# Performance work log

Hardware: AMD Instinct MI355X
Metric: run time of the kernel (lower is better)

## Reference

```python
import jax, jax.numpy as jnp
import numpy as np

D = 768       # model dim
H = 8         # heads
DH = 96       # dim per head
M = 256       # FAVOR+ random features
DEPTH = 6
B = 8
NM = 4        # n_masks
FF = 3072     # 4*dim feedforward
N = 512       # tokens = (1024/16)*(128/16)


def setup_inputs() -> dict:
    key = jax.random.key(0)
    ks = jax.random.split(key, 16)
    g = lambda k, shape: jax.random.normal(k, shape, jnp.float32) * 0.02
    return {
        "mel": jax.random.normal(ks[0], (B, 1, 1024, 128), jnp.float32),
        "patch_w": g(ks[1], (D, 1, 16, 16)),
        "patch_b": jnp.zeros((D,), jnp.float32),
        "pos_embed": g(ks[2], (1, N, D)),
        "proj": jax.random.normal(ks[3], (M, DH), jnp.float32),  # FAVOR+ projection (buffer, no grad)
        "ln1_s": jnp.ones((DEPTH, D)), "ln1_b": jnp.zeros((DEPTH, D)),
        "qkv_w": g(ks[4], (DEPTH, D, 3 * D)), "qkv_b": jnp.zeros((DEPTH, 3 * D)),
        "ao_w": g(ks[5], (DEPTH, D, D)), "ao_b": jnp.zeros((DEPTH, D)),
        "ln2_s": jnp.ones((DEPTH, D)), "ln2_b": jnp.zeros((DEPTH, D)),
        "ff1_w": g(ks[6], (DEPTH, D, FF)), "ff1_b": jnp.zeros((DEPTH, FF)),
        "ff2_w": g(ks[7], (DEPTH, FF, D)), "ff2_b": jnp.zeros((DEPTH, D)),
        "mask_w": g(ks[8], (D, NM)), "mask_b": jnp.zeros((NM,), jnp.float32),
    }


def _ln(x, s, b):
    mu = x.mean(-1, keepdims=True)
    v = ((x - mu) ** 2).mean(-1, keepdims=True)
    return (x - mu) / jnp.sqrt(v + 1e-5) * s + b


def _phi(x, proj, is_query):
    # FAVOR+ softmax-kernel feature map. x: (b,h,n,d), proj: (m,d)
    xd = x * (x.shape[-1] ** -0.25)            # d^{-1/4} data normalizer
    u = jnp.einsum('bhnd,md->bhnm', xd, proj)
    diag = 0.5 * jnp.sum(xd * xd, axis=-1, keepdims=True)
    stab = jnp.max(u, axis=-1, keepdims=True) if is_query else jnp.max(u)
    stab = jax.lax.stop_gradient(stab)          # matches .detach() in performer
    return (jnp.exp(u - diag - stab) + 1e-4) * (proj.shape[0] ** -0.5)


def reference(mel, patch_w, patch_b, pos_embed, proj, ln1_s, ln1_b, qkv_w, qkv_b,
              ao_w, ao_b, ln2_s, ln2_b, ff1_w, ff1_b, ff2_w, ff2_b, mask_w, mask_b):
    # --- frozen AudioMAE patch embed (+pos embed), under no_grad in torch ---
    x = jax.lax.conv_general_dilated(mel, patch_w, (16, 16), 'VALID',
                                     dimension_numbers=('NCHW', 'OIHW', 'NCHW'))  # (B,D,64,8)
    b = x.shape[0]
    x = x.reshape(b, D, -1).transpose(0, 2, 1) + patch_b  # (B,N,D)
    x = x + pos_embed
    x = jax.lax.stop_gradient(x)
    proj = jax.lax.stop_gradient(proj)

    def heads(t):
        return t.reshape(b, -1, H, DH).transpose(0, 2, 1, 3)  # (b,h,n,dh)

    for l in range(DEPTH):
        # --- FAVOR+ linear attention block ---
        h = _ln(x, ln1_s[l], ln1_b[l])
        qkv = h @ qkv_w[l] + qkv_b[l]
        q, k, v = (heads(t) for t in jnp.split(qkv, 3, axis=-1))
        pq = _phi(q, proj, True)
        pk = _phi(k, proj, False)
        ctx = jnp.einsum('bhnm,bhne->bhme', pk, v)       # (b,h,m,dh) linear-time kv summary
        out = jnp.einsum('bhnm,bhme->bhne', pq, ctx)
        den = jnp.einsum('bhnm,bhm->bhn', pq, pk.sum(axis=2))
        out = out / den[..., None]
        out = out.transpose(0, 2, 1, 3).reshape(b, -1, D)
        x = x + out @ ao_w[l] + ao_b[l]
        # --- feedforward block ---
        h = _ln(x, ln2_s[l], ln2_b[l])
        h = jax.nn.gelu(h @ ff1_w[l] + ff1_b[l], approximate=False)
        x = x + h @ ff2_w[l] + ff2_b[l]

    logits = x @ mask_w + mask_b              # (B,N,M)
    masks = jax.nn.sigmoid(logits)
    return masks.transpose(0, 2, 1)           # (B,M,N)
```

## Files before the change

### kernel.cpp

```cpp
#include <hip/hip_runtime.h>
#include <hip/hip_bf16.h>

typedef __bf16 bf16;
typedef __bf16 bf16x8 __attribute__((ext_vector_type(8)));
typedef float f32x4 __attribute__((ext_vector_type(4)));
typedef unsigned int u32;

#define PHI_SCALE  0.31947154f
#define DIAG_SCALE 0.05103104f
#define FEAT_SCALE 0.0625f

__device__ __forceinline__ void glds16(const bf16* g, bf16* l) {
  __builtin_amdgcn_global_load_lds(
      (const __attribute__((address_space(1))) u32*)g,
      (__attribute__((address_space(3))) u32*)l, 16, 0, 0);
}

__device__ __forceinline__ void xcd_remap(int& bx, int& by) {
  int nbx = gridDim.x, nby = gridDim.y;
  int lin = bx + nbx * by;
  int xcd = lin & 7, idx = lin >> 3;
  int mloc = nbx >> 2, nloc = nby >> 1;
  int xm = xcd & 3, xn = xcd >> 2;
  bx = xm * mloc + (idx % mloc);
  by = xn * nloc + (idx / mloc);
}

__device__ __forceinline__ int swz_scol(int lane) {
  return (((lane & 3) ^ ((lane >> 3) & 3)) * 8);
}

__device__ __forceinline__ float waveSum(float v) {
#pragma unroll
  for (int o = 32; o > 0; o >>= 1) v += __shfl_xor(v, o, 64);
  return v;
}
__device__ __forceinline__ float waveMax(float v) {
#pragma unroll
  for (int o = 32; o > 0; o >>= 1) v = fmaxf(v, __shfl_xor(v, o, 64));
  return v;
}
__device__ __forceinline__ float blockSum(float v) {
  __shared__ float tmp[4];
  v = waveSum(v);
  if ((threadIdx.x & 63) == 0) tmp[threadIdx.x >> 6] = v;
  __syncthreads();
  float r = tmp[0] + tmp[1] + tmp[2] + tmp[3];
  __syncthreads();
  return r;
}
__device__ __forceinline__ float blockMax(float v) {
  __shared__ float tmp[4];
  v = waveMax(v);
  if ((threadIdx.x & 63) == 0) tmp[threadIdx.x >> 6] = v;
  __syncthreads();
  float r = fmaxf(fmaxf(tmp[0], tmp[1]), fmaxf(tmp[2], tmp[3]));
  __syncthreads();
  return r;
}

__global__ __launch_bounds__(256) void patches_kernel(const float* __restrict__ mel,
    bf16* __restrict__ patches) {
  int blk = blockIdx.x, t = threadIdx.x;
  int b = blk >> 9, n = blk & 511;
  int r0 = (n >> 3) << 4, c0 = (n & 7) << 4;
  patches[(size_t)blk * 256 + t] =
      (bf16)mel[((size_t)b * 1024 + r0 + (t >> 4)) * 128 + c0 + (t & 15)];
}

__global__ __launch_bounds__(256) void cvt_kernel(const float* __restrict__ src,
    bf16* __restrict__ dst, int n) {
  int i = blockIdx.x * 256 + threadIdx.x;
  if (i < n) dst[i] = (bf16)src[i];
}

__device__ __forceinline__ void tile_transpose(const float* __restrict__ src,
    bf16* __restrict__ dst, int K, int N, int bx, int by) {
  __shared__ float lds[64][65];
  int n0 = bx * 64, k0 = by * 64;
  int t = threadIdx.x;
  for (int idx = t; idx < 4096; idx += 256) {
    int r = idx >> 6, c = idx & 63;
    lds[r][c] = src[(size_t)(k0 + r) * N + n0 + c];
  }
  __syncthreads();
  for (int idx = t; idx < 4096; idx += 256) {
    int r = idx >> 6, c = idx & 63;
    dst[(size_t)(n0 + r) * K + k0 + c] = (bf16)lds[c][r];
  }
}
__global__ __launch_bounds__(256) void transpose4_kernel(
    const float* __restrict__ w0, bf16* __restrict__ d0,
    const float* __restrict__ w1, bf16* __restrict__ d1,
    const float* __restrict__ w2, bf16* __restrict__ d2,
    const float* __restrict__ w3, bf16* __restrict__ d3) {
  int i = blockIdx.x;
  if (i < 432)       { tile_transpose(w0, d0, 768, 2304, i % 36, i / 36); }
  else if (i < 576)  { i -= 432;  tile_transpose(w1, d1, 768, 768, i % 12, i / 12); }
  else if (i < 1152) { i -= 576;  tile_transpose(w2, d2, 768, 3072, i % 48, i / 48);}
  else               { i -= 1152; tile_transpose(w3, d3, 3072, 768, i % 12, i / 12);}
}

__global__ __launch_bounds__(256) void ln_kernel(const float* __restrict__ x,
    const float* __restrict__ s, const float* __restrict__ bta, bf16* __restrict__ h) {
  int row = blockIdx.x;
  const float* xr = x + (size_t)row * 768;
  int t = threadIdx.x;
  float v0 = xr[t], v1 = xr[t + 256], v2 = xr[t + 512];
  float mu = blockSum(v0 + v1 + v2) * (1.f / 768.f);
  float d0 = v0 - mu, d1 = v1 - mu, d2 = v2 - mu;
  float var = blockSum(d0 * d0 + d1 * d1 + d2 * d2) * (1.f / 768.f);
  float inv = rsqrtf(var + 1e-5f);
  bf16* hr = h + (size_t)row * 768;
  hr[t]       = (bf16)(d0 * inv * s[t]       + bta[t]);
  hr[t + 256] = (bf16)(d1 * inv * s[t + 256] + bta[t + 256]);
  hr[t + 512] = (bf16)(d2 * inv * s[t + 512] + bta[t + 512]);
}

__global__ __launch_bounds__(256) void gemm128(const bf16* __restrict__ A,
    const bf16* __restrict__ B, const float* __restrict__ bias,
    bf16* __restrict__ outb, int N, int K, int mode) {
  __shared__ __attribute__((aligned(16))) bf16 lds_a[2 * 128 * 32];
  __shared__ __attribute__((aligned(16))) bf16 lds_b[2 * 128 * 32];
  int bx = blockIdx.x, by = blockIdx.y;
  xcd_remap(bx, by);
  const int t = threadIdx.x;
  const int m0 = bx * 128, n0 = by * 128;
  const int wave = t >> 6, lane = t & 63;
  const int quad = lane >> 4, id = lane & 15;
  const int wr = wave >> 1, wc = wave & 1;
  const int srow = lane >> 2, scol = swz_scol(lane);
  const bf16* pa0 = A + (size_t)(m0 + wave * 32 + srow) * K + scol;
  const bf16* pa1 = pa0 + (size_t)16 * K;
  const bf16* pb0 = B + (size_t)(n0 + wave * 32 + srow) * K + scol;
  const bf16* pb1 = pb0 + (size_t)16 * K;
  bf16* la = lds_a + wave * 1024;
  bf16* lb = lds_b + wave * 1024;
  const int sl = (quad ^ ((id >> 1) & 3)) * 8;
  f32x4 acc[4][4] = {};
  for (int k0 = 0; k0 < K; k0 += 64) {
    glds16(pa0, la);      glds16(pa1, la + 512);
    glds16(pa0 + 32, la + 4096); glds16(pa1 + 32, la + 4096 + 512);
    glds16(pb0, lb);      glds16(pb1, lb + 512);
    glds16(pb0 + 32, lb + 4096); glds16(pb1 + 32, lb + 4096 + 512);
    pa0 += 64; pa1 += 64; pb0 += 64; pb1 += 64;
    __syncthreads();
#pragma unroll
    for (int kh = 0; kh < 2; kh++) {
      bf16x8 af[4], bg[4];
#pragma unroll
      for (int i = 0; i < 4; i++)
        af[i] = *(bf16x8*)&lds_a[kh * 4096 + (wr * 64 + i * 16 + id) * 32 + sl];
#pragma unroll
      for (int j = 0; j < 4; j++)
        bg[j] = *(bf16x8*)&lds_b[kh * 4096 + (wc * 64 + j * 16 + id) * 32 + sl];
#pragma unroll
      for (int i = 0; i < 4; i++)
#pragma unroll
        for (int j = 0; j < 4; j++)
          acc[i][j] = __builtin_amdgcn_mfma_f32_16x16x32_bf16(af[i], bg[j], acc[i][j], 0, 0, 0);
    }
    __syncthreads();
  }
#pragma unroll
  for (int i = 0; i < 4; i++) {
#pragma unroll
    for (int j = 0; j < 4; j++) {
#pragma unroll
      for (int r = 0; r < 4; r++) {
        int rr = m0 + wr * 64 + i * 16 + quad * 4 + r;
        int cc = n0 + wc * 64 + j * 16 + id;
        float v = acc[i][j][r] + bias[cc];
        if (mode == 1) v = 0.5f * v * (1.0f + erff(v * 0.70710678f));
        outb[(size_t)rr * N + cc] = (bf16)v;
      }
    }
  }
}

__global__ __launch_bounds__(256) void gemm_b64(const bf16* __restrict__ A,
    const bf16* __restrict__ B, const float* __restrict__ bias,
    bf16* __restrict__ outb, float* __restrict__ xout,
    const float* __restrict__ pos, int N, int kchunk, int mode) {
  __shared__ __attribute__((aligned(16))) bf16 lds_a[2 * 128 * 32];
  __shared__ __attribute__((aligned(16))) bf16 lds_b[2 * 64 * 32];
  int bx = blockIdx.x, by = blockIdx.y;
  xcd_remap(bx, by);
  const int t = threadIdx.x;
  const int m0 = bx * 128, n0 = by * 64;
  const int kz = blockIdx.z;
  const int k_start = kz * kchunk;
  const int wave = t >> 6, lane = t & 63;
  const int quad = lane >> 4, id = lane & 15;
  const int srow = lane >> 2, scol = swz_scol(lane);
  const int K = kchunk * gridDim.z;
  const bf16* pa0 = A + (size_t)(m0 + wave * 32 + srow) * K + k_start + scol;
  const bf16* pa1 = pa0 + (size_t)16 * K;
  const bf16* pb  = B + (size_t)(n0 + wave * 16 + srow) * K + k_start + scol;
  bf16* la = lds_a + wave * 1024;
  bf16* lb = lds_b + wave * 512;
  const int sl = (quad ^ ((id >> 1) & 3)) * 8;
  f32x4 acc[2][4] = {};
  for (int k0 = 0; k0 < kchunk; k0 += 64) {
    glds16(pa0, la);      glds16(pa1, la + 512);
    glds16(pa0 + 32, la + 4096); glds16(pa1 + 32, la + 4096 + 512);
    glds16(pb, lb);       glds16(pb + 32, lb + 2048);
    pa0 += 64; pa1 += 64; pb += 64;
    __syncthreads();
#pragma unroll
    for (int kh = 0; kh < 2; kh++) {
      bf16x8 af[2], bg[4];
#pragma unroll
      for (int i = 0; i < 2; i++)
        af[i] = *(bf16x8*)&lds_a[kh * 4096 + (wave * 32 + i * 16 + id) * 32 + sl];
#pragma unroll
      for (int j = 0; j < 4; j++)
        bg[j] = *(bf16x8*)&lds_b[kh * 2048 + (j * 16 + id) * 32 + sl];
#pragma unroll
      for (int i = 0; i < 2; i++)
#pragma unroll
        for (int j = 0; j < 4; j++)
          acc[i][j] = __builtin_amdgcn_mfma_f32_16x16x32_bf16(af[i], bg[j], acc[i][j], 0, 0, 0);
    }
    __syncthreads();
  }
#pragma unroll
  for (int i = 0; i < 2; i++) {
#pragma unroll
    for (int j = 0; j < 4; j++) {
#pragma unroll
      for (int r = 0; r < 4; r++) {
        int rr = m0 + wave * 32 + i * 16 + quad * 4 + r;
        int cc = n0 + j * 16 + id;
        if (mode == 4) {
          float v = acc[i][j][r] + (kz == 0 ? bias[cc] : 0.f);
          atomicAdd(&xout[(size_t)rr * N + cc], v);
        } else {
          float v = acc[i][j][r] + bias[cc];
          if (mode == 0) {
            outb[(size_t)rr * N + cc] = (bf16)v;
          } else if (mode == 1) {
            outb[(size_t)rr * N + cc] = (bf16)(0.5f * v * (1.0f + erff(v * 0.70710678f)));
          } else {
            xout[(size_t)rr * N + cc] = v + pos[(size_t)(rr & 511) * 768 + cc];
          }
        }
      }
    }
  }
}

__global__ __launch_bounds__(256) void phi_q_kernel(const bf16* __restrict__ qkv,
    const bf16* __restrict__ proj, bf16* __restrict__ pq) {
  __shared__ __attribute__((aligned(16))) bf16 lA[3][64 * 32];
  __shared__ __attribute__((aligned(16))) bf16 lB[3][256 * 32];
  __shared__ float sqlds[64];
  const int t = threadIdx.x;
  const int nt = blockIdx.x, bh = blockIdx.y;
  const int b = bh >> 3, h = bh & 7;
  const int n0 = nt * 64;
  const bf16* Abase = qkv + ((size_t)(b * 512 + n0)) * 2304 + h * 96;
#pragma unroll
  for (int c = 0; c < 3; c++) {
    int v = c * 256 + t;
    int row = v / 12, s = v % 12;
    *(bf16x8*)&lA[s >> 2][row * 32 + (s & 3) * 8] = *(const bf16x8*)&Abase[(size_t)row * 2304 + s * 8];
  }
#pragma unroll
  for (int c = 0; c < 12; c++) {
    int v = c * 256 + t;
    int row = v / 12, s = v % 12;
    *(bf16x8*)&lB[s >> 2][row * 32 + (s & 3) * 8] = *(const bf16x8*)&proj[(size_t)row * 96 + s * 8];
  }
  __syncthreads();
  const int wave = t >> 6, lane = t & 63, quad = lane >> 4, id = lane & 15;
  f32x4 acc[16] = {};
  float sq = 0.f;
#pragma unroll
  for (int kb = 0; kb < 3; kb++) {
    bf16x8 af = *(bf16x8*)&lA[kb][(wave * 16 + id) * 32 + quad * 8];
#pragma unroll
    for (int e = 0; e < 8; e++) { float fv = (float)af[e]; sq += fv * fv; }
#pragma unroll
    for (int j = 0; j < 16; j++) {
      bf16x8 bg = *(bf16x8*)&lB[kb][(j * 16 + id) * 32 + quad * 8];
      acc[j] = __builtin_amdgcn_mfma_f32_16x16x32_bf16(af, bg, acc[j], 0, 0, 0);
    }
  }
  sq += __shfl_xor(sq, 16, 64);
  sq += __shfl_xor(sq, 32, 64);
  if (quad == 0) sqlds[wave * 16 + id] = sq;
  __syncthreads();
#pragma unroll
  for (int r = 0; r < 4; r++) {
    int rrow = quad * 4 + r;
    float dg = DIAG_SCALE * sqlds[wave * 16 + rrow];
    float mx = -1e30f;
#pragma unroll
    for (int j = 0; j < 16; j++) mx = fmaxf(mx, acc[j][r]);
    mx = fmaxf(mx, __shfl_xor(mx, 1, 64));
    mx = fmaxf(mx, __shfl_xor(mx, 2, 64));
    mx = fmaxf(mx, __shfl_xor(mx, 4, 64));
    mx = fmaxf(mx, __shfl_xor(mx, 8, 64));
    float umax = mx * PHI_SCALE;
#pragma unroll
    for (int j = 0; j < 16; j++) {
      float uu = acc[j][r] * PHI_SCALE;
      float val = (expf(uu - dg - umax) + 1e-4f) * FEAT_SCALE;
      pq[((size_t)bh * 512 + n0 + wave * 16 + rrow) * 256 + j * 16 + id] = (bf16)val;
    }
  }
}

__global__ __launch_bounds__(256) void phi_k_kernel(const bf16* __restrict__ qkv,
    const bf16* __restrict__ proj, bf16* __restrict__ prov, float* __restrict__ kbm) {
  __shared__ __attribute__((aligned(16))) bf16 lA[3][64 * 32];
  __shared__ __attribute__((aligned(16))) bf16 lB[3][256 * 32];
  __shared__ float sqlds[64];
  __shared__ float bmax4[4];
  const int t = threadIdx.x;
  const int nt = blockIdx.x, bh = blockIdx.y;
  const int b = bh >> 3, h = bh & 7;
  const int n0 = nt * 64;
  const bf16* Abase = qkv + ((size_t)(b * 512 + n0)) * 2304 + 768 + h * 96;
#pragma unroll
  for (int c = 0; c < 3; c++) {
    int v = c * 256 + t;
    int row = v / 12, s = v % 12;
    *(bf16x8*)&lA[s >> 2][row * 32 + (s & 3) * 8] = *(const bf16x8*)&Abase[(size_t)row * 2304 + s * 8];
  }
#pragma unroll
  for (int c = 0; c < 12; c++) {
    int v = c * 256 + t;
    int row = v / 12, s = v % 12;
    *(bf16x8*)&lB[s >> 2][row * 32 + (s & 3) * 8] = *(const bf16x8*)&proj[(size_t)row * 96 + s * 8];
  }
  __syncthreads();
  const int wave = t >> 6, lane = t & 63, quad = lane >> 4, id = lane & 15;
  f32x4 acc[16] = {};
  float sq = 0.f;
#pragma unroll
  for (int kb = 0; kb < 3; kb++) {
    bf16x8 af = *(bf16x8*)&lA[kb][(wave * 16 + id) * 32 + quad * 8];
#pragma unroll
    for (int e = 0; e < 8; e++) { float fv = (float)af[e]; sq += fv * fv; }
#pragma unroll
    for (int j = 0; j < 16; j++) {
      bf16x8 bg = *(bf16x8*)&lB[kb][(j * 16 + id) * 32 + quad * 8];
      acc[j] = __builtin_amdgcn_mfma_f32_16x16x32_bf16(af, bg, acc[j], 0, 0, 0);
    }
  }
  sq += __shfl_xor(sq, 16, 64);
  sq += __shfl_xor(sq, 32, 64);
  if (quad == 0) sqlds[wave * 16 + id] = sq;
  float bm = -1e30f;
#pragma unroll
  for (int j = 0; j < 16; j++)
#pragma unroll
    for (int r = 0; r < 4; r++) bm = fmaxf(bm, acc[j][r]);
  bm = waveMax(bm);
  if (lane == 0) bmax4[wave] = bm;
  __syncthreads();
  float blkmax = fmaxf(fmaxf(bmax4[0], bmax4[1]), fmaxf(bmax4[2], bmax4[3])) * PHI_SCALE;
  if (t == 0) kbm[bh * 8 + nt] = blkmax;
#pragma unroll
  for (int r = 0; r < 4; r++) {
    int rrow = quad * 4 + r;
    float dg = DIAG_SCALE * sqlds[wave * 16 + rrow];
#pragma unroll
    for (int j = 0; j < 16; j++) {
      float uu = acc[j][r] * PHI_SCALE;
      prov[((size_t)bh * 512 + n0 + wave * 16 + rrow) * 256 + j * 16 + id] =
          (bf16)expf(uu - dg - blkmax);
    }
  }
}

__global__ __launch_bounds__(256) void pkt_kernel(const bf16* __restrict__ prov,
    const float* __restrict__ kbm, bf16* __restrict__ pkT) {
  __shared__ bf16 lds[64][65];
  const int m0 = blockIdx.x * 64, nt = blockIdx.y, bh = blockIdx.z;
  const int n0 = nt * 64;
  const int t = threadIdx.x;
  float gmax = blockMax(fmaxf(kbm[t], kbm[t + 256]));
  float factor = expf(kbm[bh * 8 + nt] - gmax);
  const bf16* src = prov + ((size_t)bh * 512 + n0) * 256 + m0;
#pragma unroll
  for (int c = 0; c < 16; c++) {
    int idx = c * 256 + t; int r = idx >> 6, cc = idx & 63;
    float pv = (float)src[(size_t)r * 256 + cc];
    lds[cc][r] = (bf16)((pv * factor + 1e-4f) * FEAT_SCALE);
  }
  __syncthreads();
  bf16* dst = pkT + ((size_t)bh * 256 + m0) * 512 + n0;
#pragma unroll
  for (int c = 0; c < 16; c++) {
    int idx = c * 256 + t; int r = idx >> 6, cc = idx & 63;
    dst[(size_t)r * 512 + cc] = lds[r][cc];
  }
}

__global__ __launch_bounds__(256) void vt_kernel(const bf16* __restrict__ qkv, bf16* __restrict__ vT) {
  __shared__ bf16 lds[64][97];
  int bh = blockIdx.y, b = bh >> 3, h = bh & 7;
  int n0 = blockIdx.x * 64;
  int t = threadIdx.x;
  const bf16* src = qkv + ((size_t)b * 512 + n0) * 2304 + 1536 + h * 96;
  for (int idx = t; idx < 6144; idx += 256) {
    int r = idx / 96, c = idx % 96;
    lds[r][c] = src[(size_t)r * 2304 + c];
  }
  __syncthreads();
  bf16* dst = vT + (size_t)bh * 96 * 512 + n0;
  for (int idx = t; idx < 6144; idx += 256) {
    int e = idx >> 6, nn = idx & 63;
    dst[(size_t)e * 512 + nn] = lds[nn][e];
  }
}

__global__ __launch_bounds__(256) void ctx_gemm(const bf16* __restrict__ pkT,
    const bf16* __restrict__ vT, bf16* __restrict__ ctxT, float* __restrict__ ksum) {
  __shared__ __attribute__((aligned(16))) bf16 lds_a[64 * 40];
  __shared__ __attribute__((aligned(16))) bf16 lds_b[96 * 40];
  const int t = threadIdx.x;
  const int bh = blockIdx.y, m0 = blockIdx.x * 64;
  const bf16* A = pkT + (size_t)bh * 256 * 512;
  const bf16* B = vT + (size_t)bh * 96 * 512;
  const int wave = t >> 6, lane = t & 63;
  const int quad = lane >> 4, id = lane & 15;
  const int row = t >> 2, kof = (t & 3) * 8;
  f32x4 acc[6] = {};
  float ks = 0.f;
  for (int k0 = 0; k0 < 512; k0 += 32) {
    *(bf16x8*)&lds_a[row * 40 + kof] = *(const bf16x8*)&A[(size_t)(m0 + row) * 512 + k0 + kof];
    for (int idx = t; idx < 384; idx += 256) {
      int r2 = idx >> 2, k2 = (idx & 3) * 8;
      *(bf16x8*)&lds_b[r2 * 40 + k2] = *(const bf16x8*)&B[(size_t)r2 * 512 + k0 + k2];
    }
    __syncthreads();
    bf16x8 af = *(bf16x8*)&lds_a[(wave * 16 + id) * 40 + quad * 8];
#pragma unroll
    for (int e = 0; e < 8; e++) ks += (float)af[e];
#pragma unroll
    for (int j = 0; j < 6; j++) {
      bf16x8 bg = *(bf16x8*)&lds_b[(j * 16 + id) * 40 + quad * 8];
      acc[j] = __builtin_amdgcn_mfma_f32_16x16x32_bf16(af, bg, acc[j], 0, 0, 0);
    }
    __syncthreads();
  }
  ks += __shfl_xor(ks, 16, 64);
  ks += __shfl_xor(ks, 32, 64);
  if (quad == 0) ksum[bh * 256 + m0 + wave * 16 + id] = ks;
#pragma unroll
  for (int j = 0; j < 6; j++)
#pragma unroll
    for (int r = 0; r < 4; r++) {
      int e = j * 16 + id;
      int m = m0 + wave * 16 + quad * 4 + r;
      ctxT[((size_t)bh * 96 + e) * 256 + m] = (bf16)acc[j][r];
    }
}

__global__ __launch_bounds__(256) void out_gemm(const bf16* __restrict__ pq,
    const bf16* __restrict__ ctxT, const float* __restrict__ ksum, bf16* __restrict__ attn) {
  __shared__ __attribute__((aligned(16))) bf16 lds_a[64 * 40];
  __shared__ __attribute__((aligned(16))) bf16 lds_b[96 * 40];
  __shared__ float den_lds[64];
  const int t = threadIdx.x;
  const int bh = blockIdx.y, m0 = blockIdx.x * 64;
  const int b = bh >> 3, h = bh & 7;
  const bf16* A = pq + (size_t)bh * 512 * 256;
  const bf16* B = ctxT + (size_t)bh * 96 * 256;
  const int wave = t >> 6, lane = t & 63;
  const int quad = lane >> 4, id = lane & 15;
  const int row = t >> 2, kof = (t & 3) * 8;
  f32x4 acc[6] = {};
  float den = 0.f;
  for (int k0 = 0; k0 < 256; k0 += 32) {
    *(bf16x8*)&lds_a[row * 40 + kof] = *(const bf16x8*)&A[(size_t)(m0 + row) * 256 + k0 + kof];
    for (int idx = t; idx < 384; idx += 256) {
      int r2 = idx >> 2, k2 = (idx & 3) * 8;
      *(bf16x8*)&lds_b[r2 * 40 + k2] = *(const bf16x8*)&B[(size_t)r2 * 256 + k0 + k2];
    }
    __syncthreads();
    bf16x8 af = *(bf16x8*)&lds_a[(wave * 16 + id) * 40 + quad * 8];
    const f32x4* kp = (const f32x4*)(ksum + bh * 256 + k0 + quad * 8);
    f32x4 k0v = kp[0], k1v = kp[1];
#pragma unroll
    for (int e = 0; e < 4; e++) den += (float)af[e] * k0v[e];
#pragma unroll
    for (int e = 0; e < 4; e++) den += (float)af[e + 4] * k1v[e];
#pragma unroll
    for (int j = 0; j < 6; j++) {
      bf16x8 bg = *(bf16x8*)&lds_b[(j * 16 + id) * 40 + quad * 8];
      acc[j] = __builtin_amdgcn_mfma_f32_16x16x32_bf16(af, bg, acc[j], 0, 0, 0);
    }
    __syncthreads();
  }
  den += __shfl_xor(den, 16, 64);
  den += __shfl_xor(den, 32, 64);
  if (quad == 0) den_lds[wave * 16 + id] = den;
  __syncthreads();
#pragma unroll
  for (int j = 0; j < 6; j++)
#pragma unroll
    for (int r = 0; r < 4; r++) {
      int e = j * 16 + id;
      int n = m0 + wave * 16 + quad * 4 + r;
      float v = acc[j][r] / fmaxf(den_lds[wave * 16 + quad * 4 + r], 1e-30f);
      attn[((size_t)(b * 512 + n)) * 768 + h * 96 + e] = (bf16)v;
    }
}

__global__ __launch_bounds__(256) void mask_kernel(const float* __restrict__ x,
    const float* __restrict__ mw, const float* __restrict__ mb, float* __restrict__ out) {
  int row = blockIdx.x * 4 + (threadIdx.x >> 6);
  int lane = threadIdx.x & 63;
  int b = row >> 9, n = row & 511;
  const float* xr = x + (size_t)row * 768;
  float a0 = 0, a1 = 0, a2 = 0, a3 = 0;
  for (int d = lane; d < 768; d += 64) {
    float xv = xr[d];
    a0 += xv * mw[d * 4 + 0];
    a1 += xv * mw[d * 4 + 1];
    a2 += xv * mw[d * 4 + 2];
    a3 += xv * mw[d * 4 + 3];
  }
  a0 = waveSum(a0); a1 = waveSum(a1); a2 = waveSum(a2); a3 = waveSum(a3);
  if (lane == 0) {
    out[((size_t)b * 4 + 0) * 512 + n] = 1.f / (1.f + expf(-(a0 + mb[0])));
    out[((size_t)b * 4 + 1) * 512 + n] = 1.f / (1.f + expf(-(a1 + mb[1])));
    out[((size_t)b * 4 + 2) * 512 + n] = 1.f / (1.f + expf(-(a2 + mb[2])));
    out[((size_t)b * 4 + 3) * 512 + n] = 1.f / (1.f + expf(-(a3 + mb[3])));
  }
}

extern "C" void kernel_launch(void* const* d_in, const int* in_sizes, int n_in,
                              void* d_out, int out_size, void* d_ws, size_t ws_size,
                              hipStream_t stream) {
  const float* mel     = (const float*)d_in[0];
  const float* patch_w = (const float*)d_in[1];
  const float* patch_b = (const float*)d_in[2];
  const float* pos     = (const float*)d_in[3];
  const float* proj    = (const float*)d_in[4];
  const float* ln1_s   = (const float*)d_in[5];
  const float* ln1_b   = (const float*)d_in[6];
  const float* qkv_w   = (const float*)d_in[7];
  const float* qkv_b   = (const float*)d_in[8];
  const float* ao_w    = (const float*)d_in[9];
  const float* ao_b    = (const float*)d_in[10];
  const float* ln2_s   = (const float*)d_in[11];
  const float* ln2_b   = (const float*)d_in[12];
  const float* ff1_w   = (const float*)d_in[13];
  const float* ff1_b   = (const float*)d_in[14];
  const float* ff2_w   = (const float*)d_in[15];
  const float* ff2_b   = (const float*)d_in[16];
  const float* mask_w  = (const float*)d_in[17];
  const float* mask_b  = (const float*)d_in[18];

  char* ws = (char*)d_ws;
  size_t off = 0;
  auto alloc = [&](size_t bytes) { void* p = ws + off; off += (bytes + 255) & ~(size_t)255; return p; };
  float* x     = (float*)alloc(4096ull * 768 * 4);
  bf16* h      = (bf16*)alloc(4096ull * 768 * 2);
  bf16* qkv    = (bf16*)alloc(4096ull * 2304 * 2);
  bf16* wtq    = (bf16*)alloc(2304ull * 768 * 2);
  bf16* wta    = (bf16*)alloc(768ull * 768 * 2);
  bf16* wtf1   = (bf16*)alloc(3072ull * 768 * 2);
  bf16* wtf2   = (bf16*)alloc(768ull * 3072 * 2);
  bf16* patches= (bf16*)alloc(4096ull * 256 * 2);
  bf16* pwb    = (bf16*)alloc(768ull * 256 * 2);
  bf16* projb  = (bf16*)alloc(256ull * 96 * 2);
  bf16* pq     = (bf16*)alloc(8388608ull * 2);
  bf16* prov   = (bf16*)alloc(8388608ull * 2);
  bf16* pkT    = (bf16*)alloc(8388608ull * 2);
  bf16* vT     = (bf16*)alloc(64ull * 96 * 512 * 2);
  bf16* ctxT   = (bf16*)alloc(64ull * 96 * 256 * 2);
  float* ksum  = (float*)alloc(64ull * 256 * 4);
  float* kbm   = (float*)alloc(512ull * 4);
  float* gmax  = (float*)alloc(256);
  bf16* attn   = (bf16*)alloc(4096ull * 768 * 2);
  bf16* ffh    = (bf16*)alloc(4096ull * 3072 * 2);
  if (ws_size < off) return;

  patches_kernel<<<4096, 256, 0, stream>>>(mel, patches);
  cvt_kernel<<<768, 256, 0, stream>>>(patch_w, pwb, 196608);
  cvt_kernel<<<96, 256, 0, stream>>>(proj, projb, 24576);
  gemm_b64<<<dim3(32, 12), 256, 0, stream>>>(patches, pwb, patch_b, nullptr, x, pos,
                                             768, 256, 3);

  for (int l = 0; l < 6; l++) {
    transpose4_kernel<<<1728, 256, 0, stream>>>(
        qkv_w + (size_t)l * 768 * 2304, wtq,
        ao_w + (size_t)l * 768 * 768, wta,
        ff1_w + (size_t)l * 768 * 3072, wtf1,
        ff2_w + (size_t)l * 3072 * 768, wtf2);

    ln_kernel<<<4096, 256, 0, stream>>>(x, ln1_s + l * 768, ln1_b + l * 768, h);
    gemm128<<<dim3(32, 18), 256, 0, stream>>>(h, wtq, qkv_b + l * 2304, qkv, 2304, 768, 0);

    phi_q_kernel<<<dim3(8, 64), 256, 0, stream>>>(qkv, projb, pq);
    phi_k_kernel<<<dim3(8, 64), 256, 0, stream>>>(qkv, projb, prov, kbm);
    pkt_kernel<<<dim3(4, 8, 64), 256, 0, stream>>>(prov, kbm, pkT);
    vt_kernel<<<dim3(8, 64), 256, 0, stream>>>(qkv, vT);
    ctx_gemm<<<dim3(4, 64), 256, 0, stream>>>(pkT, vT, ctxT, ksum);
    out_gemm<<<dim3(8, 64), 256, 0, stream>>>(pq, ctxT, ksum, attn);
    gemm_b64<<<dim3(32, 12, 2), 256, 0, stream>>>(attn, wta, ao_b + l * 768, nullptr, x,
                                                  nullptr, 768, 384, 4);

    ln_kernel<<<4096, 256, 0, stream>>>(x, ln2_s + l * 768, ln2_b + l * 768, h);
    gemm128<<<dim3(32, 24), 256, 0, stream>>>(h, wtf1, ff1_b + l * 3072, ffh, 3072, 768, 1);
    gemm_b64<<<dim3(32, 12, 2), 256, 0, stream>>>(ffh, wtf2, ff2_b + l * 768, nullptr, x,
                                                  nullptr, 768, 1536, 4);
  }

  mask_kernel<<<1024, 256, 0, stream>>>(x, mask_w, mask_b, (float*)d_out);
}
```

Baseline: 1.473 ms.

## Fuse phi_k transpose into phi_k, apply global-max rescale in ctx_gemm, raise split-K

phi_k_kernel now transposes its unnormalized exp features through LDS and writes pkT directly, which removes the separate pkt_kernel pass and the prov buffer. The global key-max rescale and the 1e-4 offset are applied in ctx_gemm as the A operand is loaded, and the key sums are computed from the rescaled values. The attention-output and FF2 GEMMs also go from split-K 2 to 4. The costs are extra per-element work inside ctx_gemm, a second bf16 rounding of the key features, scalar 2-byte stores in phi_k, and more atomic or partial-sum traffic from the higher split-K.

```diff
diff --git a/kernel.cpp b/kernel.cpp
--- a/kernel.cpp
+++ b/kernel.cpp
@@ -313,7 +313,7 @@
 }
 
 __global__ __launch_bounds__(256) void phi_k_kernel(const bf16* __restrict__ qkv,
-    const bf16* __restrict__ proj, bf16* __restrict__ prov, float* __restrict__ kbm) {
+    const bf16* __restrict__ proj, bf16* __restrict__ pkT, float* __restrict__ kbm) {
   __shared__ __attribute__((aligned(16))) bf16 lA[3][64 * 32];
   __shared__ __attribute__((aligned(16))) bf16 lB[3][256 * 32];
   __shared__ float sqlds[64];
@@ -363,40 +363,24 @@
   __syncthreads();
   float blkmax = fmaxf(fmaxf(bmax4[0], bmax4[1]), fmaxf(bmax4[2], bmax4[3])) * PHI_SCALE;
   if (t == 0) kbm[bh * 8 + nt] = blkmax;
+  bf16* sT = &lB[0][0];
 #pragma unroll
   for (int r = 0; r < 4; r++) {
-    int rrow = quad * 4 + r;
-    float dg = DIAG_SCALE * sqlds[wave * 16 + rrow];
+    int rrow = wave * 16 + quad * 4 + r;
+    float dg = DIAG_SCALE * sqlds[rrow];
 #pragma unroll
     for (int j = 0; j < 16; j++) {
       float uu = acc[j][r] * PHI_SCALE;
-      prov[((size_t)bh * 512 + n0 + wave * 16 + rrow) * 256 + j * 16 + id] =
-          (bf16)expf(uu - dg - blkmax);
-    }
-  }
-}
-
-__global__ __launch_bounds__(256) void pkt_kernel(const bf16* __restrict__ prov,
-    const float* __restrict__ kbm, bf16* __restrict__ pkT) {
-  __shared__ bf16 lds[64][65];
-  const int m0 = blockIdx.x * 64, nt = blockIdx.y, bh = blockIdx.z;
-  const int n0 = nt * 64;
-  const int t = threadIdx.x;
-  float gmax = blockMax(fmaxf(kbm[t], kbm[t + 256]));
-  float factor = expf(kbm[bh * 8 + nt] - gmax);
-  const bf16* src = prov + ((size_t)bh * 512 + n0) * 256 + m0;
-#pragma unroll
-  for (int c = 0; c < 16; c++) {
-    int idx = c * 256 + t; int r = idx >> 6, cc = idx & 63;
-    float pv = (float)src[(size_t)r * 256 + cc];
-    lds[cc][r] = (bf16)((pv * factor + 1e-4f) * FEAT_SCALE);
-  }
-  __syncthreads();
-  bf16* dst = pkT + ((size_t)bh * 256 + m0) * 512 + n0;
-#pragma unroll
-  for (int c = 0; c < 16; c++) {
-    int idx = c * 256 + t; int r = idx >> 6, cc = idx & 63;
-    dst[(size_t)r * 512 + cc] = lds[r][cc];
+      sT[(j * 16 + id) * 66 + rrow] = (bf16)expf(uu - dg - blkmax);
+    }
+  }
+  __syncthreads();
+  bf16* dst = pkT + ((size_t)bh * 256) * 512 + n0;
+#pragma unroll
+  for (int it = 0; it < 64; it++) {
+    int idx = it * 256 + t;
+    int m = idx >> 6, n = idx & 63;
+    dst[(size_t)m * 512 + n] = sT[m * 66 + n];
   }
 }
 
@@ -419,7 +403,8 @@
 }
 
 __global__ __launch_bounds__(256) void ctx_gemm(const bf16* __restrict__ pkT,
-    const bf16* __restrict__ vT, bf16* __restrict__ ctxT, float* __restrict__ ksum) {
+    const bf16* __restrict__ vT, const float* __restrict__ kbm,
+    bf16* __restrict__ ctxT, float* __restrict__ ksum) {
   __shared__ __attribute__((aligned(16))) bf16 lds_a[64 * 40];
   __shared__ __attribute__((aligned(16))) bf16 lds_b[96 * 40];
   const int t = threadIdx.x;
@@ -429,9 +414,12 @@
   const int wave = t >> 6, lane = t & 63;
   const int quad = lane >> 4, id = lane & 15;
   const int row = t >> 2, kof = (t & 3) * 8;
+  float gm = blockMax(fmaxf(kbm[t], kbm[t + 256]));
   f32x4 acc[6] = {};
   float ks = 0.f;
+  const float offc = 1e-4f * FEAT_SCALE;
   for (int k0 = 0; k0 < 512; k0 += 32) {
+    float fs = expf(kbm[bh * 8 + (k0 >> 6)] - gm) * FEAT_SCALE;
     *(bf16x8*)&lds_a[row * 40 + kof] = *(const bf16x8*)&A[(size_t)(m0 + row) * 512 + k0 + kof];
     for (int idx = t; idx < 384; idx += 256) {
       int r2 = idx >> 2, k2 = (idx & 3) * 8;
@@ -439,12 +427,17 @@
     }
     __syncthreads();
     bf16x8 af = *(bf16x8*)&lds_a[(wave * 16 + id) * 40 + quad * 8];
-#pragma unroll
-    for (int e = 0; e < 8; e++) ks += (float)af[e];
+    bf16x8 afs;
+#pragma unroll
+    for (int e = 0; e < 8; e++) {
+      float f = (float)af[e] * fs + offc;
+      ks += f;
+      afs[e] = (bf16)f;
+    }
 #pragma unroll
     for (int j = 0; j < 6; j++) {
       bf16x8 bg = *(bf16x8*)&lds_b[(j * 16 + id) * 40 + quad * 8];
-      acc[j] = __builtin_amdgcn_mfma_f32_16x16x32_bf16(af, bg, acc[j], 0, 0, 0);
+      acc[j] = __builtin_amdgcn_mfma_f32_16x16x32_bf16(afs, bg, acc[j], 0, 0, 0);
     }
     __syncthreads();
   }
@@ -572,13 +565,11 @@
   bf16* pwb    = (bf16*)alloc(768ull * 256 * 2);
   bf16* projb  = (bf16*)alloc(256ull * 96 * 2);
   bf16* pq     = (bf16*)alloc(8388608ull * 2);
-  bf16* prov   = (bf16*)alloc(8388608ull * 2);
   bf16* pkT    = (bf16*)alloc(8388608ull * 2);
   bf16* vT     = (bf16*)alloc(64ull * 96 * 512 * 2);
   bf16* ctxT   = (bf16*)alloc(64ull * 96 * 256 * 2);
   float* ksum  = (float*)alloc(64ull * 256 * 4);
   float* kbm   = (float*)alloc(512ull * 4);
-  float* gmax  = (float*)alloc(256);
   bf16* attn   = (bf16*)alloc(4096ull * 768 * 2);
   bf16* ffh    = (bf16*)alloc(4096ull * 3072 * 2);
   if (ws_size < off) return;
@@ -600,18 +591,17 @@
     gemm128<<<dim3(32, 18), 256, 0, stream>>>(h, wtq, qkv_b + l * 2304, qkv, 2304, 768, 0);
 
     phi_q_kernel<<<dim3(8, 64), 256, 0, stream>>>(qkv, projb, pq);
-    phi_k_kernel<<<dim3(8, 64), 256, 0, stream>>>(qkv, projb, prov, kbm);
-    pkt_kernel<<<dim3(4, 8, 64), 256, 0, stream>>>(prov, kbm, pkT);
+    phi_k_kernel<<<dim3(8, 64), 256, 0, stream>>>(qkv, projb, pkT, kbm);
     vt_kernel<<<dim3(8, 64), 256, 0, stream>>>(qkv, vT);
-    ctx_gemm<<<dim3(4, 64), 256, 0, stream>>>(pkT, vT, ctxT, ksum);
+    ctx_gemm<<<dim3(4, 64), 256, 0, stream>>>(pkT, vT, kbm, ctxT, ksum);
     out_gemm<<<dim3(8, 64), 256, 0, stream>>>(pq, ctxT, ksum, attn);
-    gemm_b64<<<dim3(32, 12, 2), 256, 0, stream>>>(attn, wta, ao_b + l * 768, nullptr, x,
-                                                  nullptr, 768, 384, 4);
+    gemm_b64<<<dim3(32, 12, 4), 256, 0, stream>>>(attn, wta, ao_b + l * 768, nullptr, x,
+                                                  nullptr, 768, 192, 4);
 
     ln_kernel<<<4096, 256, 0, stream>>>(x, ln2_s + l * 768, ln2_b + l * 768, h);
     gemm128<<<dim3(32, 24), 256, 0, stream>>>(h, wtf1, ff1_b + l * 3072, ffh, 3072, 768, 1);
-    gemm_b64<<<dim3(32, 12, 2), 256, 0, stream>>>(ffh, wtf2, ff2_b + l * 768, nullptr, x,
-                                                  nullptr, 768, 1536, 4);
+    gemm_b64<<<dim3(32, 12, 4), 256, 0, stream>>>(ffh, wtf2, ff2_b + l * 768, nullptr, x,
+                                                  nullptr, 768, 768, 4);
   }
 
   mask_kernel<<<1024, 256, 0, stream>>>(x, mask_w, mask_b, (float*)d_out);
```

Result: slower. 1.700 ms (+15.4%).
